# Performance work log

Hardware: AMD Instinct MI355X
Metric: run time of the kernel (lower is better)

Reference implementation:

```python
import jax, jax.numpy as jnp
import numpy as np
import math

HIDDEN = 1024
NUM_LAYERS = 24
INIT_RANGE = 0.02


def setup_inputs() -> dict:
    key = jax.random.key(0)
    k1, k2 = jax.random.split(key)
    B, S, H = 4, 4096, HIDDEN
    hidden_states = jax.random.normal(k1, (B, S, H), dtype=jnp.float32)
    std = INIT_RANGE / math.sqrt(2.0 * NUM_LAYERS * H)
    # queries weight: [H, H], applied as F.linear => x @ W^T
    W_q = jax.random.normal(k2, (H, H), dtype=jnp.float32) * std
    return {"hidden_states": hidden_states, "W_q": W_q}


def reference(hidden_states, W_q):
    # queries = F.linear(x, W) = x @ W^T          [B, S, H]
    q = jnp.einsum('bsh,oh->bso', hidden_states, W_q)
    # pre_attn = Q @ K^T where K = x             [B, S, S]
    pre_attn = jnp.einsum('bso,bto->bst', q, hidden_states)
    # attention = pre_attn @ V where V = x       [B, S, H]
    attention = jnp.einsum('bst,bth->bsh', pre_attn, hidden_states)
    return attention
```

## Files before the change

### kernel.cpp

```cpp
#include <hip/hip_runtime.h>
#include <hip/hip_bf16.h>
#include <stdint.h>

#define H_DIM 1024
#define S_DIM 4096
#define B_DIM 4
#define NTRI 36

typedef __bf16 bf16x8 __attribute__((ext_vector_type(8)));
typedef float f32x4 __attribute__((ext_vector_type(4)));
typedef unsigned short u16x4 __attribute__((ext_vector_type(4)));

__device__ __forceinline__ unsigned short f2bf(float f) {
    union { float f; uint32_t u; } v; v.f = f;
    uint32_t u = v.u;
    uint32_t r = (u + 0x7FFFu + ((u >> 16) & 1u)) >> 16;
    return (unsigned short)r;
}
__device__ __forceinline__ float bf2f(unsigned short u) {
    union { uint32_t u; float f; } v; v.u = (uint32_t)u << 16; return v.f;
}

__device__ __forceinline__ void wg_barrier() {
    asm volatile("s_barrier" ::: "memory");
}

__global__ void cast_x_kernel(const float* __restrict__ X,
                              unsigned short* __restrict__ Xb,
                              unsigned short* __restrict__ XT) {
    __shared__ float tile[32][33];
    const int b  = blockIdx.z;
    const int h0 = blockIdx.x * 32;
    const int s0 = blockIdx.y * 32;
    const int tx = threadIdx.x;
    const int ty = threadIdx.y;
    const float* src = X + ((size_t)b * S_DIM + s0) * H_DIM + h0;
#pragma unroll
    for (int i = 0; i < 4; ++i) {
        int s = ty + 8 * i;
        float v = src[(size_t)s * H_DIM + tx];
        tile[s][tx] = v;
        Xb[((size_t)b * S_DIM + s0 + s) * H_DIM + h0 + tx] = f2bf(v);
    }
    __syncthreads();
#pragma unroll
    for (int i = 0; i < 4; ++i) {
        int hh = ty + 8 * i;
        XT[((size_t)b * H_DIM + h0 + hh) * S_DIM + s0 + tx] = f2bf(tile[tx][hh]);
    }
}

__global__ void cast_w_kernel(const float* __restrict__ W,
                              unsigned short* __restrict__ WT) {
    __shared__ float tile[32][33];
    const int b0 = blockIdx.x * 32;
    const int o0 = blockIdx.y * 32;
    const int tx = threadIdx.x;
    const int ty = threadIdx.y;
#pragma unroll
    for (int i = 0; i < 4; ++i) {
        int o = ty + 8 * i;
        tile[o][tx] = W[(size_t)(o0 + o) * H_DIM + b0 + tx];
    }
    __syncthreads();
#pragma unroll
    for (int i = 0; i < 4; ++i) {
        int bb = ty + 8 * i;
        WT[(size_t)(b0 + bb) * H_DIM + o0 + tx] = f2bf(tile[tx][bb]);
    }
}

template <int NSPLIT>
__global__ void reduce_cast_u16_kernel(const unsigned short* __restrict__ P,
                                       unsigned short* __restrict__ Out,
                                       size_t sSplit) {
    size_t i = ((size_t)blockIdx.x * blockDim.x + threadIdx.x) * 4;
    float s0 = 0.f, s1 = 0.f, s2 = 0.f, s3 = 0.f;
#pragma unroll
    for (int sp = 0; sp < NSPLIT; ++sp) {
        u16x4 u = *(const u16x4*)&P[(size_t)sp * sSplit + i];
        s0 += bf2f(u[0]); s1 += bf2f(u[1]); s2 += bf2f(u[2]); s3 += bf2f(u[3]);
    }
    u16x4 o;
    o[0] = f2bf(s0); o[1] = f2bf(s1); o[2] = f2bf(s2); o[3] = f2bf(s3);
    *(u16x4*)&Out[i] = o;
}

template <int NS>
__global__ __launch_bounds__(256)
void reduce_sym_kernel(const unsigned short* __restrict__ P,
                       unsigned short* __restrict__ G) {
    __shared__ unsigned short t[128 * 129];
    const int tid  = threadIdx.x;
    const int tile = blockIdx.x;
    const int b    = blockIdx.y;
    int ti = 0;
    while ((ti + 1) * (ti + 2) / 2 <= tile) ++ti;
    const int tj = tile - ti * (ti + 1) / 2;
    unsigned short* Gb = G + (size_t)b * (H_DIM * H_DIM);
    const unsigned short* Pb = P + ((size_t)(b * NS) * NTRI + tile) * 16384;
#pragma unroll
    for (int it = 0; it < 16; ++it) {
        int i = it * 1024 + tid * 4;
        float s0 = 0.f, s1 = 0.f, s2 = 0.f, s3 = 0.f;
#pragma unroll
        for (int sp = 0; sp < NS; ++sp) {
            u16x4 u = *(const u16x4*)&Pb[(size_t)sp * (NTRI * 16384) + i];
            s0 += bf2f(u[0]); s1 += bf2f(u[1]); s2 += bf2f(u[2]); s3 += bf2f(u[3]);
        }
        u16x4 o;
        o[0] = f2bf(s0); o[1] = f2bf(s1); o[2] = f2bf(s2); o[3] = f2bf(s3);
        int r = i >> 7, c = i & 127;
        *(u16x4*)&Gb[(size_t)(ti * 128 + r) * H_DIM + tj * 128 + c] = o;
        t[r * 129 + c + 0] = o[0];
        t[r * 129 + c + 1] = o[1];
        t[r * 129 + c + 2] = o[2];
        t[r * 129 + c + 3] = o[3];
    }
    __syncthreads();
#pragma unroll
    for (int it = 0; it < 16; ++it) {
        int j = it * 1024 + tid * 4;
        int rr = j >> 7, cc = j & 127;
        u16x4 o;
        o[0] = t[(cc + 0) * 129 + rr];
        o[1] = t[(cc + 1) * 129 + rr];
        o[2] = t[(cc + 2) * 129 + rr];
        o[3] = t[(cc + 3) * 129 + rr];
        *(u16x4*)&Gb[(size_t)(tj * 128 + rr) * H_DIM + ti * 128 + cc] = o;
    }
}

template <typename OutT, int NSPLIT, bool TRI, bool SWAPXY>
__global__ __launch_bounds__(256, 2)
void gemm_bt_kernel(const unsigned short* __restrict__ A,
                    const unsigned short* __restrict__ Bt,
                    OutT* __restrict__ C,
                    int K, int lda, int ldb, int ldc,
                    size_t sA, size_t sB, size_t sC, size_t sSplit) {
    __shared__ __align__(16) union Sh {
        unsigned short stage[2][2][8192];
        float epi[4][1088];
    } sh;

    const int tid  = threadIdx.x;
    const int w    = tid >> 6;
    const int lane = tid & 63;
    const int wm   = w & 1;
    const int wn   = w >> 1;
    const int q    = lane >> 4;
    const int col  = lane & 15;

    int tileM, tileN, tileIdx = 0;
    if constexpr (TRI) {
        tileIdx = (int)blockIdx.x;
        int ti = 0;
        while ((ti + 1) * (ti + 2) / 2 <= tileIdx) ++ti;
        int tj = tileIdx - ti * (ti + 1) / 2;
        tileM = ti * 128;
        tileN = tj * 128;
    } else if constexpr (SWAPXY) {
        tileM = blockIdx.x * 128;
        tileN = blockIdx.y * 128;
    } else {
        tileN = blockIdx.x * 128;
        tileM = blockIdx.y * 128;
    }
    const int bz   = blockIdx.z / NSPLIT;
    const int sp   = blockIdx.z % NSPLIT;
    const int Ksub = K / NSPLIT;

    const unsigned short* Ab = A + sA * bz + (size_t)sp * Ksub;
    const unsigned short* Bb = Bt + sB * bz + (size_t)sp * Ksub;

    const unsigned short* gA[4];
    const unsigned short* gB[4];
    int ldsOff[4];
#pragma unroll
    for (int i = 0; i < 4; ++i) {
        int chunk = (w << 2) | i;
        int m  = ((chunk & 1) << 6) | lane;
        int k8 = chunk >> 1;
        gA[i] = Ab + (size_t)(tileM + m) * lda + k8 * 8;
        gB[i] = Bb + (size_t)(tileN + m) * ldb + k8 * 8;
        ldsOff[i] = chunk * 512;
    }

    auto stage = [&](int buf) {
#pragma unroll
        for (int i = 0; i < 4; ++i) {
            __builtin_amdgcn_global_load_lds(
                (const __attribute__((address_space(1))) void*)gA[i],
                (__attribute__((address_space(3))) void*)&sh.stage[buf][0][ldsOff[i]],
                16, 0, 0);
            __builtin_amdgcn_global_load_lds(
                (const __attribute__((address_space(1))) void*)gB[i],
                (__attribute__((address_space(3))) void*)&sh.stage[buf][1][ldsOff[i]],
                16, 0, 0);
            gA[i] += 64;
            gB[i] += 64;
        }
    };

    f32x4 acc[4][4];
#pragma unroll
    for (int r = 0; r < 4; ++r)
#pragma unroll
        for (int c = 0; c < 4; ++c)
            acc[r][c] = (f32x4){0.f, 0.f, 0.f, 0.f};

    const int T = Ksub >> 6;

    stage(0);
    if (T > 1) stage(1);

    for (int t = 0; t < T; ++t) {
        if (t + 1 < T) asm volatile("s_waitcnt vmcnt(8)" ::: "memory");
        else           asm volatile("s_waitcnt vmcnt(0)" ::: "memory");
        wg_barrier();

        const int cur = t & 1;
        const unsigned short* As = sh.stage[cur][0];
        const unsigned short* Bs = sh.stage[cur][1];
#pragma unroll
        for (int kc = 0; kc < 2; ++kc) {
            bf16x8 av[4], bv[4];
#pragma unroll
            for (int r = 0; r < 4; ++r)
                av[r] = *(const bf16x8*)&As[(((kc * 4 + q) * 128) + wm * 64 + r * 16 + col) * 8];
#pragma unroll
            for (int c = 0; c < 4; ++c)
                bv[c] = *(const bf16x8*)&Bs[(((kc * 4 + q) * 128) + wn * 64 + c * 16 + col) * 8];
#pragma unroll
            for (int r = 0; r < 4; ++r)
#pragma unroll
                for (int c = 0; c < 4; ++c)
                    acc[r][c] = __builtin_amdgcn_mfma_f32_16x16x32_bf16(
                        av[r], bv[c], acc[r][c], 0, 0, 0);
        }

        wg_barrier();
        if (t + 2 < T) stage(cur);
    }

    OutT* Cb;
    int ldcl, rowBase, colBase;
    if constexpr (TRI) {
        Cb = C + ((size_t)blockIdx.z * NTRI + tileIdx) * 16384;
        ldcl = 128; rowBase = 0; colBase = 0;
    } else {
        Cb = C + sC * bz + sSplit * sp;
        ldcl = ldc; rowBase = tileM; colBase = tileN;
    }

    float* lws = sh.epi[w];
    const int lr = lane >> 4;
    const int lc = lane & 15;
#pragma unroll
    for (int r = 0; r < 4; ++r) {
        __syncthreads();
#pragma unroll
        for (int c = 0; c < 4; ++c)
#pragma unroll
            for (int v = 0; v < 4; ++v)
                lws[(q * 4 + v) * 68 + c * 16 + col] = acc[r][c][v];
        __syncthreads();
#pragma unroll
        for (int p = 0; p < 4; ++p) {
            f32x4 t = *(const f32x4*)&lws[(p * 4 + lr) * 68 + lc * 4];
            int row  = rowBase + wm * 64 + r * 16 + p * 4 + lr;
            int colg = colBase + wn * 64 + lc * 4;
            if constexpr (sizeof(OutT) == 2) {
                u16x4 u;
                u[0] = f2bf(t[0]); u[1] = f2bf(t[1]);
                u[2] = f2bf(t[2]); u[3] = f2bf(t[3]);
                *(u16x4*)&Cb[(size_t)row * ldcl + colg] = u;
            } else {
                *(f32x4*)&Cb[(size_t)row * ldcl + colg] = t;
            }
        }
    }
}

extern "C" void kernel_launch(void* const* d_in, const int* in_sizes, int n_in,
                              void* d_out, int out_size, void* d_ws, size_t ws_size,
                              hipStream_t stream) {
    const float* X = (const float*)d_in[0];
    const float* W = (const float*)d_in[1];
    float* out = (float*)d_out;

    char* ws = (char*)d_ws;
    unsigned short* Xb = (unsigned short*)(ws);
    unsigned short* XT = (unsigned short*)(ws + 33554432);
    unsigned short* WT = (unsigned short*)(ws + 67108864);
    unsigned short* G  = (unsigned short*)(ws + 69206016);
    unsigned short* MT = (unsigned short*)(ws + 77594624);
    unsigned short* Gpart  = (unsigned short*)(ws + 85983232);
    unsigned short* MTpart = (unsigned short*)(ws + 85983232);

    cast_x_kernel<<<dim3(H_DIM / 32, S_DIM / 32, B_DIM), dim3(32, 8), 0, stream>>>(X, Xb, XT);
    cast_w_kernel<<<dim3(H_DIM / 32, H_DIM / 32, 1), dim3(32, 8), 0, stream>>>(W, WT);

    gemm_bt_kernel<unsigned short, 4, true, false><<<dim3(NTRI, 1, B_DIM * 4), 256, 0, stream>>>(
        XT, XT, Gpart, S_DIM, S_DIM, S_DIM, 128,
        (size_t)H_DIM * S_DIM, (size_t)H_DIM * S_DIM, 0, 0);
    reduce_sym_kernel<4><<<dim3(NTRI, B_DIM), 256, 0, stream>>>(Gpart, G);

    gemm_bt_kernel<unsigned short, 2, false, false><<<dim3(8, 8, B_DIM * 2), 256, 0, stream>>>(
        G, WT, MTpart, H_DIM, H_DIM, H_DIM, H_DIM,
        (size_t)H_DIM * H_DIM, (size_t)0, (size_t)H_DIM * H_DIM,
        (size_t)B_DIM * H_DIM * H_DIM);
    reduce_cast_u16_kernel<2><<<dim3(B_DIM * H_DIM * H_DIM / 4 / 256), 256, 0, stream>>>(
        MTpart, MT, (size_t)B_DIM * H_DIM * H_DIM);

    gemm_bt_kernel<float, 1, false, true><<<dim3(S_DIM / 128, 8, B_DIM), 256, 0, stream>>>(
        Xb, MT, out, H_DIM, H_DIM, H_DIM, H_DIM,
        (size_t)S_DIM * H_DIM, (size_t)H_DIM * H_DIM, (size_t)S_DIM * H_DIM, 0);
}
```

Before: 282.5 us.

## Replace GEMM with 256x256-tile, 4-stage pipelined kernel and drop symmetric Gram path

```diff
diff --git a/kernel.cpp b/kernel.cpp
--- a/kernel.cpp
+++ b/kernel.cpp
@@ -5,7 +5,6 @@
 #define H_DIM 1024
 #define S_DIM 4096
 #define B_DIM 4
-#define NTRI 36
 
 typedef __bf16 bf16x8 __attribute__((ext_vector_type(8)));
 typedef float f32x4 __attribute__((ext_vector_type(4)));
@@ -23,6 +22,14 @@
 
 __device__ __forceinline__ void wg_barrier() {
     asm volatile("s_barrier" ::: "memory");
+}
+
+template <int IMM>
+__device__ __forceinline__ bf16x8 ds_read_b128_imm(unsigned addr) {
+    bf16x8 r;
+    asm volatile("ds_read_b128 %0, %1 offset:%2"
+                 : "=v"(r) : "v"(addr), "i"(IMM));
+    return r;
 }
 
 __global__ void cast_x_kernel(const float* __restrict__ X,
@@ -86,62 +93,14 @@
     *(u16x4*)&Out[i] = o;
 }
 
-template <int NS>
-__global__ __launch_bounds__(256)
-void reduce_sym_kernel(const unsigned short* __restrict__ P,
-                       unsigned short* __restrict__ G) {
-    __shared__ unsigned short t[128 * 129];
-    const int tid  = threadIdx.x;
-    const int tile = blockIdx.x;
-    const int b    = blockIdx.y;
-    int ti = 0;
-    while ((ti + 1) * (ti + 2) / 2 <= tile) ++ti;
-    const int tj = tile - ti * (ti + 1) / 2;
-    unsigned short* Gb = G + (size_t)b * (H_DIM * H_DIM);
-    const unsigned short* Pb = P + ((size_t)(b * NS) * NTRI + tile) * 16384;
-#pragma unroll
-    for (int it = 0; it < 16; ++it) {
-        int i = it * 1024 + tid * 4;
-        float s0 = 0.f, s1 = 0.f, s2 = 0.f, s3 = 0.f;
-#pragma unroll
-        for (int sp = 0; sp < NS; ++sp) {
-            u16x4 u = *(const u16x4*)&Pb[(size_t)sp * (NTRI * 16384) + i];
-            s0 += bf2f(u[0]); s1 += bf2f(u[1]); s2 += bf2f(u[2]); s3 += bf2f(u[3]);
-        }
-        u16x4 o;
-        o[0] = f2bf(s0); o[1] = f2bf(s1); o[2] = f2bf(s2); o[3] = f2bf(s3);
-        int r = i >> 7, c = i & 127;
-        *(u16x4*)&Gb[(size_t)(ti * 128 + r) * H_DIM + tj * 128 + c] = o;
-        t[r * 129 + c + 0] = o[0];
-        t[r * 129 + c + 1] = o[1];
-        t[r * 129 + c + 2] = o[2];
-        t[r * 129 + c + 3] = o[3];
-    }
-    __syncthreads();
-#pragma unroll
-    for (int it = 0; it < 16; ++it) {
-        int j = it * 1024 + tid * 4;
-        int rr = j >> 7, cc = j & 127;
-        u16x4 o;
-        o[0] = t[(cc + 0) * 129 + rr];
-        o[1] = t[(cc + 1) * 129 + rr];
-        o[2] = t[(cc + 2) * 129 + rr];
-        o[3] = t[(cc + 3) * 129 + rr];
-        *(u16x4*)&Gb[(size_t)(tj * 128 + rr) * H_DIM + ti * 128 + cc] = o;
-    }
-}
-
-template <typename OutT, int NSPLIT, bool TRI, bool SWAPXY>
-__global__ __launch_bounds__(256, 2)
-void gemm_bt_kernel(const unsigned short* __restrict__ A,
+template <typename OutT, int NSPLIT>
+__global__ __launch_bounds__(512, 2)
+void gemm_q4_kernel(const unsigned short* __restrict__ A,
                     const unsigned short* __restrict__ Bt,
                     OutT* __restrict__ C,
                     int K, int lda, int ldb, int ldc,
                     size_t sA, size_t sB, size_t sC, size_t sSplit) {
-    __shared__ __align__(16) union Sh {
-        unsigned short stage[2][2][8192];
-        float epi[4][1088];
-    } sh;
+    extern __shared__ char smem_raw[];
 
     const int tid  = threadIdx.x;
     const int w    = tid >> 6;
@@ -151,132 +110,142 @@
     const int q    = lane >> 4;
     const int col  = lane & 15;
 
-    int tileM, tileN, tileIdx = 0;
-    if constexpr (TRI) {
-        tileIdx = (int)blockIdx.x;
-        int ti = 0;
-        while ((ti + 1) * (ti + 2) / 2 <= tileIdx) ++ti;
-        int tj = tileIdx - ti * (ti + 1) / 2;
-        tileM = ti * 128;
-        tileN = tj * 128;
-    } else if constexpr (SWAPXY) {
-        tileM = blockIdx.x * 128;
-        tileN = blockIdx.y * 128;
-    } else {
-        tileN = blockIdx.x * 128;
-        tileM = blockIdx.y * 128;
-    }
+    const int tileM = blockIdx.x * 256;
+    const int tileN = blockIdx.y * 256;
     const int bz   = blockIdx.z / NSPLIT;
     const int sp   = blockIdx.z % NSPLIT;
     const int Ksub = K / NSPLIT;
+    const int T    = Ksub >> 5;
 
     const unsigned short* Ab = A + sA * bz + (size_t)sp * Ksub;
     const unsigned short* Bb = Bt + sB * bz + (size_t)sp * Ksub;
 
-    const unsigned short* gA[4];
-    const unsigned short* gB[4];
-    int ldsOff[4];
-#pragma unroll
-    for (int i = 0; i < 4; ++i) {
-        int chunk = (w << 2) | i;
-        int m  = ((chunk & 1) << 6) | lane;
-        int k8 = chunk >> 1;
-        gA[i] = Ab + (size_t)(tileM + m) * lda + k8 * 8;
-        gB[i] = Bb + (size_t)(tileN + m) * ldb + k8 * 8;
-        ldsOff[i] = chunk * 512;
-    }
-
-    auto stage = [&](int buf) {
-#pragma unroll
-        for (int i = 0; i < 4; ++i) {
+    auto lds3 = (__attribute__((address_space(3))) char*)&smem_raw[0];
+    const unsigned ldsBase = (unsigned)(size_t)lds3;
+
+    const unsigned aBase = ldsBase + (unsigned)(q * 4096 + wm * 2048 + col * 16);
+    const unsigned bBase = ldsBase + 16384u + (unsigned)(q * 4096 + wn * 1024 + col * 16);
+
+    const unsigned short* srcA[2];
+    const unsigned short* srcB[2];
+    int dstOf[2];
+#pragma unroll
+    for (int j = 0; j < 2; ++j) {
+        int c = 2 * w + j;
+        int k8l = c >> 2, r64 = c & 3;
+        srcA[j] = Ab + (size_t)(tileM + r64 * 64 + lane) * lda + k8l * 8;
+        srcB[j] = Bb + (size_t)(tileN + r64 * 64 + lane) * ldb + k8l * 8;
+        dstOf[j] = (k8l * 256 + r64 * 64) * 16;
+    }
+
+    auto stageA = [&](int buf) {
+#pragma unroll
+        for (int j = 0; j < 2; ++j) {
             __builtin_amdgcn_global_load_lds(
-                (const __attribute__((address_space(1))) void*)gA[i],
-                (__attribute__((address_space(3))) void*)&sh.stage[buf][0][ldsOff[i]],
+                (const __attribute__((address_space(1))) void*)srcA[j],
+                (__attribute__((address_space(3))) void*)(lds3 + buf * 32768 + dstOf[j]),
                 16, 0, 0);
-            __builtin_amdgcn_global_load_lds(
-                (const __attribute__((address_space(1))) void*)gB[i],
-                (__attribute__((address_space(3))) void*)&sh.stage[buf][1][ldsOff[i]],
-                16, 0, 0);
-            gA[i] += 64;
-            gB[i] += 64;
+            srcA[j] += 32;
         }
     };
-
-    f32x4 acc[4][4];
-#pragma unroll
-    for (int r = 0; r < 4; ++r)
+    auto stageB = [&](int buf) {
+#pragma unroll
+        for (int j = 0; j < 2; ++j) {
+            __builtin_amdgcn_global_load_lds(
+                (const __attribute__((address_space(1))) void*)srcB[j],
+                (__attribute__((address_space(3))) void*)(lds3 + buf * 32768 + 16384 + dstOf[j]),
+                16, 0, 0);
+            srcB[j] += 32;
+        }
+    };
+
+    f32x4 acc[8][4];
+#pragma unroll
+    for (int r = 0; r < 8; ++r)
 #pragma unroll
         for (int c = 0; c < 4; ++c)
             acc[r][c] = (f32x4){0.f, 0.f, 0.f, 0.f};
 
-    const int T = Ksub >> 6;
-
-    stage(0);
-    if (T > 1) stage(1);
-
-    for (int t = 0; t < T; ++t) {
-        if (t + 1 < T) asm volatile("s_waitcnt vmcnt(8)" ::: "memory");
-        else           asm volatile("s_waitcnt vmcnt(0)" ::: "memory");
-        wg_barrier();
-
-        const int cur = t & 1;
-        const unsigned short* As = sh.stage[cur][0];
-        const unsigned short* Bs = sh.stage[cur][1];
-#pragma unroll
-        for (int kc = 0; kc < 2; ++kc) {
-            bf16x8 av[4], bv[4];
-#pragma unroll
-            for (int r = 0; r < 4; ++r)
-                av[r] = *(const bf16x8*)&As[(((kc * 4 + q) * 128) + wm * 64 + r * 16 + col) * 8];
-#pragma unroll
-            for (int c = 0; c < 4; ++c)
-                bv[c] = *(const bf16x8*)&Bs[(((kc * 4 + q) * 128) + wn * 64 + c * 16 + col) * 8];
-#pragma unroll
-            for (int r = 0; r < 4; ++r)
-#pragma unroll
-                for (int c = 0; c < 4; ++c)
-                    acc[r][c] = __builtin_amdgcn_mfma_f32_16x16x32_bf16(
-                        av[r], bv[c], acc[r][c], 0, 0, 0);
-        }
-
-        wg_barrier();
-        if (t + 2 < T) stage(cur);
-    }
-
-    OutT* Cb;
-    int ldcl, rowBase, colBase;
-    if constexpr (TRI) {
-        Cb = C + ((size_t)blockIdx.z * NTRI + tileIdx) * 16384;
-        ldcl = 128; rowBase = 0; colBase = 0;
-    } else {
-        Cb = C + sC * bz + sSplit * sp;
-        ldcl = ldc; rowBase = tileM; colBase = tileN;
-    }
-
-    float* lws = sh.epi[w];
+    stageA(0); stageB(0);
+    stageA(1); stageB(1);
+    stageA(2); stageB(2);
+    asm volatile("s_waitcnt vmcnt(8)" ::: "memory");
+    wg_barrier();
+
+    for (int n = 0; n < T; ++n) {
+        const unsigned aAddr = aBase + (unsigned)((n & 3) << 15);
+        const unsigned bAddr = bBase + (unsigned)((n & 3) << 15);
+        const int nbuf = (n + 3) & 3;
+        bf16x8 av[4], bv[4];
+
+        av[0] = ds_read_b128_imm<0>(aAddr);
+        av[1] = ds_read_b128_imm<256>(aAddr);
+        av[2] = ds_read_b128_imm<512>(aAddr);
+        av[3] = ds_read_b128_imm<768>(aAddr);
+        bv[0] = ds_read_b128_imm<0>(bAddr);
+        bv[1] = ds_read_b128_imm<256>(bAddr);
+        bv[2] = ds_read_b128_imm<512>(bAddr);
+        bv[3] = ds_read_b128_imm<768>(bAddr);
+        if (n + 3 < T) stageA(nbuf);
+        wg_barrier();
+        asm volatile("s_waitcnt lgkmcnt(0)" ::: "memory");
+        __builtin_amdgcn_sched_barrier(0);
+        __builtin_amdgcn_s_setprio(1);
+#pragma unroll
+        for (int mf = 0; mf < 4; ++mf)
+#pragma unroll
+            for (int nf = 0; nf < 4; ++nf)
+                acc[mf][nf] = __builtin_amdgcn_mfma_f32_16x16x32_bf16(
+                    av[mf], bv[nf], acc[mf][nf], 0, 0, 0);
+        __builtin_amdgcn_s_setprio(0);
+        wg_barrier();
+
+        av[0] = ds_read_b128_imm<1024>(aAddr);
+        av[1] = ds_read_b128_imm<1280>(aAddr);
+        av[2] = ds_read_b128_imm<1536>(aAddr);
+        av[3] = ds_read_b128_imm<1792>(aAddr);
+        if (n + 3 < T) stageB(nbuf);
+        if (n < T - 3)       asm volatile("s_waitcnt vmcnt(8)" ::: "memory");
+        else if (n == T - 3) asm volatile("s_waitcnt vmcnt(4)" ::: "memory");
+        else                 asm volatile("s_waitcnt vmcnt(0)" ::: "memory");
+        wg_barrier();
+        asm volatile("s_waitcnt lgkmcnt(0)" ::: "memory");
+        __builtin_amdgcn_sched_barrier(0);
+        __builtin_amdgcn_s_setprio(1);
+#pragma unroll
+        for (int mf = 0; mf < 4; ++mf)
+#pragma unroll
+            for (int nf = 0; nf < 4; ++nf)
+                acc[4 + mf][nf] = __builtin_amdgcn_mfma_f32_16x16x32_bf16(
+                    av[mf], bv[nf], acc[4 + mf][nf], 0, 0, 0);
+        __builtin_amdgcn_s_setprio(0);
+        wg_barrier();
+    }
+
+    OutT* Cb = C + sC * bz + sSplit * sp;
+    __syncthreads();
+    float* lws = (float*)(smem_raw) + (size_t)w * 1088;
     const int lr = lane >> 4;
     const int lc = lane & 15;
 #pragma unroll
-    for (int r = 0; r < 4; ++r) {
-        __syncthreads();
-#pragma unroll
-        for (int c = 0; c < 4; ++c)
+    for (int mf = 0; mf < 8; ++mf) {
+#pragma unroll
+        for (int nf = 0; nf < 4; ++nf)
 #pragma unroll
             for (int v = 0; v < 4; ++v)
-                lws[(q * 4 + v) * 68 + c * 16 + col] = acc[r][c][v];
-        __syncthreads();
+                lws[(q * 4 + v) * 68 + nf * 16 + col] = acc[mf][nf][v];
 #pragma unroll
         for (int p = 0; p < 4; ++p) {
             f32x4 t = *(const f32x4*)&lws[(p * 4 + lr) * 68 + lc * 4];
-            int row  = rowBase + wm * 64 + r * 16 + p * 4 + lr;
-            int colg = colBase + wn * 64 + lc * 4;
+            int row  = tileM + wm * 128 + mf * 16 + p * 4 + lr;
+            int colg = tileN + wn * 64 + lc * 4;
             if constexpr (sizeof(OutT) == 2) {
                 u16x4 u;
                 u[0] = f2bf(t[0]); u[1] = f2bf(t[1]);
                 u[2] = f2bf(t[2]); u[3] = f2bf(t[3]);
-                *(u16x4*)&Cb[(size_t)row * ldcl + colg] = u;
+                *(u16x4*)&Cb[(size_t)row * ldc + colg] = u;
             } else {
-                *(f32x4*)&Cb[(size_t)row * ldcl + colg] = t;
+                *(f32x4*)&Cb[(size_t)row * ldc + colg] = t;
             }
         }
     }
@@ -298,22 +267,22 @@
     unsigned short* Gpart  = (unsigned short*)(ws + 85983232);
     unsigned short* MTpart = (unsigned short*)(ws + 85983232);
 
+    const size_t sBH = (size_t)B_DIM * H_DIM * H_DIM;
+
     cast_x_kernel<<<dim3(H_DIM / 32, S_DIM / 32, B_DIM), dim3(32, 8), 0, stream>>>(X, Xb, XT);
     cast_w_kernel<<<dim3(H_DIM / 32, H_DIM / 32, 1), dim3(32, 8), 0, stream>>>(W, WT);
 
-    gemm_bt_kernel<unsigned short, 4, true, false><<<dim3(NTRI, 1, B_DIM * 4), 256, 0, stream>>>(
-        XT, XT, Gpart, S_DIM, S_DIM, S_DIM, 128,
-        (size_t)H_DIM * S_DIM, (size_t)H_DIM * S_DIM, 0, 0);
-    reduce_sym_kernel<4><<<dim3(NTRI, B_DIM), 256, 0, stream>>>(Gpart, G);
-
-    gemm_bt_kernel<unsigned short, 2, false, false><<<dim3(8, 8, B_DIM * 2), 256, 0, stream>>>(
+    gemm_q4_kernel<unsigned short, 4><<<dim3(4, 4, B_DIM * 4), 512, 131072, stream>>>(
+        XT, XT, Gpart, S_DIM, S_DIM, S_DIM, H_DIM,
+        (size_t)H_DIM * S_DIM, (size_t)H_DIM * S_DIM, (size_t)H_DIM * H_DIM, sBH);
+    reduce_cast_u16_kernel<4><<<dim3(sBH / 4 / 256), 256, 0, stream>>>(Gpart, G, sBH);
+
+    gemm_q4_kernel<unsigned short, 4><<<dim3(4, 4, B_DIM * 4), 512, 131072, stream>>>(
         G, WT, MTpart, H_DIM, H_DIM, H_DIM, H_DIM,
-        (size_t)H_DIM * H_DIM, (size_t)0, (size_t)H_DIM * H_DIM,
-        (size_t)B_DIM * H_DIM * H_DIM);
-    reduce_cast_u16_kernel<2><<<dim3(B_DIM * H_DIM * H_DIM / 4 / 256), 256, 0, stream>>>(
-        MTpart, MT, (size_t)B_DIM * H_DIM * H_DIM);
-
-    gemm_bt_kernel<float, 1, false, true><<<dim3(S_DIM / 128, 8, B_DIM), 256, 0, stream>>>(
+        (size_t)H_DIM * H_DIM, (size_t)0, (size_t)H_DIM * H_DIM, sBH);
+    reduce_cast_u16_kernel<4><<<dim3(sBH / 4 / 256), 256, 0, stream>>>(MTpart, MT, sBH);
+
+    gemm_q4_kernel<float, 1><<<dim3(S_DIM / 256, H_DIM / 256, B_DIM), 512, 131072, stream>>>(
         Xb, MT, out, H_DIM, H_DIM, H_DIM, H_DIM,
         (size_t)S_DIM * H_DIM, (size_t)H_DIM * H_DIM, (size_t)S_DIM * H_DIM, 0);
 }
```

New measurement: 264.6 us. 6.4% less time.
